# Kernel tuning notes

Hardware: AMD Instinct MI355X
Metric: run time of the kernel (lower is better)

The kernel has to match this reference:

```python
import jax, jax.numpy as jnp
import numpy as np

B, T, I, H, O = 4096, 256, 16, 32, 1


def setup_inputs() -> dict:
    key = jax.random.key(0)
    ks = jax.random.split(key, 8)
    s_ih = 1.0 / np.sqrt(H)
    x = jax.random.normal(ks[0], (B, T, I), dtype=jnp.float32)
    # PyTorch nn.LSTM params: gate order [i, f, g, o], uniform(-1/sqrt(H), 1/sqrt(H))
    W_ih = jax.random.uniform(ks[1], (4 * H, I), minval=-s_ih, maxval=s_ih, dtype=jnp.float32)
    W_hh = jax.random.uniform(ks[2], (4 * H, H), minval=-s_ih, maxval=s_ih, dtype=jnp.float32)
    b_ih = jax.random.uniform(ks[3], (4 * H,), minval=-s_ih, maxval=s_ih, dtype=jnp.float32)
    b_hh = jax.random.uniform(ks[4], (4 * H,), minval=-s_ih, maxval=s_ih, dtype=jnp.float32)
    W_fc = jax.random.uniform(ks[5], (O, H), minval=-s_ih, maxval=s_ih, dtype=jnp.float32)
    b_fc = jax.random.uniform(ks[6], (O,), minval=-s_ih, maxval=s_ih, dtype=jnp.float32)
    return {"x": x, "W_ih": W_ih, "W_hh": W_hh, "b_ih": b_ih, "b_hh": b_hh,
            "W_fc": W_fc, "b_fc": b_fc}


def _lstm_last_hidden(x, W_ih, W_hh, b_ih, b_hh):
    # Precompute input contributions for all timesteps: [T, B, 4H]
    xg = (jnp.einsum('bti,gi->btg', x, W_ih) + b_ih + b_hh).transpose(1, 0, 2)
    h0 = jnp.zeros((x.shape[0], W_hh.shape[1]), dtype=x.dtype)
    c0 = jnp.zeros_like(h0)

    def step(carry, xg_t):
        h, c = carry
        gates = xg_t + h @ W_hh.T  # [B, 4H]
        i, f, g, o = jnp.split(gates, 4, axis=-1)
        i = jax.nn.sigmoid(i)
        f = jax.nn.sigmoid(f)
        g = jnp.tanh(g)
        o = jax.nn.sigmoid(o)
        c = f * c + i * g
        h = o * jnp.tanh(c)
        return (h, c), None

    (h_last, _), _ = jax.lax.scan(step, (h0, c0), xg)
    return h_last


def reference(x, W_ih, W_hh, b_ih, b_hh, W_fc, b_fc):
    h_last = _lstm_last_hidden(x, W_ih, W_hh, b_ih, b_hh)
    # Dropout is identity in eval mode
    return h_last @ W_fc.T + b_fc  # [B, O]
```

## Files before the change

### kernel.cpp

```cpp
#include <hip/hip_runtime.h>

#define B_ 4096
#define T_ 256
#define I_ 16
#define H_ 32

typedef _Float16 f16x4 __attribute__((ext_vector_type(4)));
typedef _Float16 f16x8 __attribute__((ext_vector_type(8)));
typedef float    f32x4 __attribute__((ext_vector_type(4)));

#define MSIG  (-1.442695041f)
#define MTANH (-2.885390082f)

__global__ __launch_bounds__(128, 1)
void lstm_mfma2(const float* __restrict__ x,
                const float* __restrict__ Wih,
                const float* __restrict__ Whh,
                const float* __restrict__ bih,
                const float* __restrict__ bhh,
                const float* __restrict__ Wfc,
                const float* __restrict__ bfc,
                float* __restrict__ out)
{
    __shared__ __align__(16) _Float16 hbuf[2][16][40];

    const int tid  = threadIdx.x;
    const int wave = tid >> 6;
    const int l    = tid & 63;
    const int lr   = l & 15;
    const int lg   = l >> 4;
    const int b0   = blockIdx.x * 16;

    f16x8 whhA[4];
    f16x8 wihA[4];
    float mb[4][4];
#pragma unroll
    for (int q = 0; q < 4; ++q) {
        const int rowA = q * 32 + wave * 16 + lr;
        const float* ph = Whh + rowA * H_ + lg * 8;
#pragma unroll
        for (int k = 0; k < 8; ++k) whhA[q][k] = (_Float16)ph[k];
        const float* pi = Wih + rowA * I_ + (lg & 1) * 8;
#pragma unroll
        for (int k = 0; k < 8; ++k)
            wihA[q][k] = (lg < 2) ? (_Float16)pi[k] : (_Float16)0.0f;
        const float m = (q == 2) ? MTANH : MSIG;
#pragma unroll
        for (int r = 0; r < 4; ++r) {
            const int rowC = q * 32 + wave * 16 + lg * 4 + r;
            mb[q][r] = m * (bih[rowC] + bhh[rowC]);
        }
    }

    for (int i = tid; i < 2 * 16 * 40; i += 128)
        ((_Float16*)hbuf)[i] = (_Float16)0.0f;
    __syncthreads();

    float c0 = 0.f, c1 = 0.f, c2 = 0.f, c3 = 0.f;

    const float* xbase = x + (size_t)(b0 + lr) * (T_ * I_) + (lg & 1) * 8;
    f16x8 xf[8];
#pragma unroll
    for (int k = 0; k < 8; ++k) {
        const float4 u0 = *reinterpret_cast<const float4*>(xbase + k * I_);
        const float4 u1 = *reinterpret_cast<const float4*>(xbase + k * I_ + 4);
        f16x8 w;
        w[0] = (_Float16)u0.x; w[1] = (_Float16)u0.y;
        w[2] = (_Float16)u0.z; w[3] = (_Float16)u0.w;
        w[4] = (_Float16)u1.x; w[5] = (_Float16)u1.y;
        w[6] = (_Float16)u1.z; w[7] = (_Float16)u1.w;
        xf[k] = w;
    }

    const f32x4 zf = {0.f, 0.f, 0.f, 0.f};

    for (int tb = 0; tb < 32; ++tb) {
#pragma unroll
        for (int tt = 0; tt < 8; ++tt) {
            const f16x8 xB = xf[tt];
            if (tb < 31) {
                const float* nx = xbase + ((tb + 1) * 8 + tt) * I_;
                const float4 u0 = *reinterpret_cast<const float4*>(nx);
                const float4 u1 = *reinterpret_cast<const float4*>(nx + 4);
                f16x8 w;
                w[0] = (_Float16)u0.x; w[1] = (_Float16)u0.y;
                w[2] = (_Float16)u0.z; w[3] = (_Float16)u0.w;
                w[4] = (_Float16)u1.x; w[5] = (_Float16)u1.y;
                w[6] = (_Float16)u1.z; w[7] = (_Float16)u1.w;
                xf[tt] = w;
            }

            const f16x8 hB = *reinterpret_cast<const f16x8*>(&hbuf[tt & 1][lr][lg * 8]);

            f32x4 a0 = __builtin_amdgcn_mfma_f32_16x16x32_f16(wihA[0], xB, zf, 0, 0, 0);
            f32x4 a1 = __builtin_amdgcn_mfma_f32_16x16x32_f16(wihA[1], xB, zf, 0, 0, 0);
            f32x4 a2 = __builtin_amdgcn_mfma_f32_16x16x32_f16(wihA[2], xB, zf, 0, 0, 0);
            f32x4 a3 = __builtin_amdgcn_mfma_f32_16x16x32_f16(wihA[3], xB, zf, 0, 0, 0);
            a0 = __builtin_amdgcn_mfma_f32_16x16x32_f16(whhA[0], hB, a0, 0, 0, 0);
            a1 = __builtin_amdgcn_mfma_f32_16x16x32_f16(whhA[1], hB, a1, 0, 0, 0);
            a2 = __builtin_amdgcn_mfma_f32_16x16x32_f16(whhA[2], hB, a2, 0, 0, 0);
            a3 = __builtin_amdgcn_mfma_f32_16x16x32_f16(whhA[3], hB, a3, 0, 0, 0);

            float si[4], sf[4], tg[4], so[4];
#pragma unroll
            for (int r = 0; r < 4; ++r) {
                si[r] = __builtin_amdgcn_rcpf(1.0f + __builtin_amdgcn_exp2f(__fmaf_rn(MSIG,  a0[r], mb[0][r])));
                sf[r] = __builtin_amdgcn_rcpf(1.0f + __builtin_amdgcn_exp2f(__fmaf_rn(MSIG,  a1[r], mb[1][r])));
                tg[r] = __fmaf_rn(2.0f, __builtin_amdgcn_rcpf(1.0f + __builtin_amdgcn_exp2f(__fmaf_rn(MTANH, a2[r], mb[2][r]))), -1.0f);
                so[r] = __builtin_amdgcn_rcpf(1.0f + __builtin_amdgcn_exp2f(__fmaf_rn(MSIG,  a3[r], mb[3][r])));
            }

            c0 = __fmaf_rn(sf[0], c0, si[0] * tg[0]);
            c1 = __fmaf_rn(sf[1], c1, si[1] * tg[1]);
            c2 = __fmaf_rn(sf[2], c2, si[2] * tg[2]);
            c3 = __fmaf_rn(sf[3], c3, si[3] * tg[3]);
            const float t0 = __fmaf_rn(2.0f, __builtin_amdgcn_rcpf(1.0f + __builtin_amdgcn_exp2f(MTANH * c0)), -1.0f);
            const float t1 = __fmaf_rn(2.0f, __builtin_amdgcn_rcpf(1.0f + __builtin_amdgcn_exp2f(MTANH * c1)), -1.0f);
            const float t2 = __fmaf_rn(2.0f, __builtin_amdgcn_rcpf(1.0f + __builtin_amdgcn_exp2f(MTANH * c2)), -1.0f);
            const float t3 = __fmaf_rn(2.0f, __builtin_amdgcn_rcpf(1.0f + __builtin_amdgcn_exp2f(MTANH * c3)), -1.0f);
            const float h0 = so[0] * t0, h1 = so[1] * t1, h2 = so[2] * t2, h3 = so[3] * t3;

            f16x4 hv;
            hv[0] = (_Float16)h0; hv[1] = (_Float16)h1;
            hv[2] = (_Float16)h2; hv[3] = (_Float16)h3;
            *reinterpret_cast<f16x4*>(&hbuf[(tt + 1) & 1][lr][wave * 16 + lg * 4]) = hv;

            __syncthreads();
        }
    }

    if (tid < 64) {
        const f16x8 hL = *reinterpret_cast<const f16x8*>(&hbuf[0][lr][lg * 8]);
        const float* pw = Wfc + lg * 8;
        float p = 0.f;
#pragma unroll
        for (int k = 0; k < 8; ++k) p += (float)hL[k] * pw[k];
        p += __shfl_xor(p, 16, 64);
        p += __shfl_xor(p, 32, 64);
        if (lg == 0) out[b0 + lr] = p + bfc[0];
    }
}

extern "C" void kernel_launch(void* const* d_in, const int* in_sizes, int n_in,
                              void* d_out, int out_size, void* d_ws, size_t ws_size,
                              hipStream_t stream) {
    const float* x   = (const float*)d_in[0];
    const float* Wih = (const float*)d_in[1];
    const float* Whh = (const float*)d_in[2];
    const float* bih = (const float*)d_in[3];
    const float* bhh = (const float*)d_in[4];
    const float* Wfc = (const float*)d_in[5];
    const float* bfc = (const float*)d_in[6];
    float* out = (float*)d_out;

    dim3 grid(B_ / 16);
    dim3 block(128);
    hipLaunchKernelGGL(lstm_mfma2, grid, block, 0, stream,
                       x, Wih, Whh, bih, bhh, Wfc, bfc, out);
}
```

Before: 265.5 us.

## Run each LSTM batch tile in one wave, keeping hidden state in registers

Each block now has a single wave that computes all 128 gate rows for 16 batch elements. The gate rows are permuted so that the MFMA output layout matches the B-operand layout of the next step's h. This removes the shared-memory hidden buffer and the per-timestep __syncthreads. The bias is also folded into the MFMA accumulator initialisation. In exchange each wave issues twice the MFMAs and activation math per step, and the block count per CU halves in thread terms, which could lengthen the serial per-step critical path.

```diff
diff --git a/kernel.cpp b/kernel.cpp
--- a/kernel.cpp
+++ b/kernel.cpp
@@ -5,74 +5,85 @@
 #define I_ 16
 #define H_ 32
 
-typedef _Float16 f16x4 __attribute__((ext_vector_type(4)));
 typedef _Float16 f16x8 __attribute__((ext_vector_type(8)));
 typedef float    f32x4 __attribute__((ext_vector_type(4)));
 
 #define MSIG  (-1.442695041f)
 #define MTANH (-2.885390082f)
 
-__global__ __launch_bounds__(128, 1)
-void lstm_mfma2(const float* __restrict__ x,
-                const float* __restrict__ Wih,
-                const float* __restrict__ Whh,
-                const float* __restrict__ bih,
-                const float* __restrict__ bhh,
-                const float* __restrict__ Wfc,
-                const float* __restrict__ bfc,
-                float* __restrict__ out)
+__device__ __forceinline__ float sigm_(float a) {
+    return __builtin_amdgcn_rcpf(1.0f + __builtin_amdgcn_exp2f(MSIG * a));
+}
+__device__ __forceinline__ float tanh_(float a) {
+    return __fmaf_rn(2.0f, __builtin_amdgcn_rcpf(1.0f + __builtin_amdgcn_exp2f(MTANH * a)), -1.0f);
+}
+
+__global__ __launch_bounds__(64, 1)
+void lstm_wave(const float* __restrict__ x,
+               const float* __restrict__ Wih,
+               const float* __restrict__ Whh,
+               const float* __restrict__ bih,
+               const float* __restrict__ bhh,
+               const float* __restrict__ Wfc,
+               const float* __restrict__ bfc,
+               float* __restrict__ out)
 {
-    __shared__ __align__(16) _Float16 hbuf[2][16][40];
+    const int l  = threadIdx.x & 63;
+    const int lr = l & 15;
+    const int lg = l >> 4;
+    const int b0 = blockIdx.x * 16;
 
-    const int tid  = threadIdx.x;
-    const int wave = tid >> 6;
-    const int l    = tid & 63;
-    const int lr   = l & 15;
-    const int lg   = l >> 4;
-    const int b0   = blockIdx.x * 16;
-
-    f16x8 whhA[4];
-    f16x8 wihA[4];
-    float mb[4][4];
+    f16x8 whhA[4][2];
+    f16x8 wihA[4][2];
+    f32x4 biasC[4][2];
+    const int jA0 = ((lr >> 2) * 8) + (lr & 3);
 #pragma unroll
     for (int q = 0; q < 4; ++q) {
-        const int rowA = q * 32 + wave * 16 + lr;
-        const float* ph = Whh + rowA * H_ + lg * 8;
 #pragma unroll
-        for (int k = 0; k < 8; ++k) whhA[q][k] = (_Float16)ph[k];
-        const float* pi = Wih + rowA * I_ + (lg & 1) * 8;
+        for (int p = 0; p < 2; ++p) {
+            const int row = q * 32 + jA0 + p * 4;
+            const float* ph = Whh + row * H_ + lg * 8;
+            f16x8 w;
 #pragma unroll
-        for (int k = 0; k < 8; ++k)
-            wihA[q][k] = (lg < 2) ? (_Float16)pi[k] : (_Float16)0.0f;
-        const float m = (q == 2) ? MTANH : MSIG;
+            for (int k = 0; k < 8; ++k) w[k] = (_Float16)ph[k];
+            whhA[q][p] = w;
+            const float* pi = Wih + row * I_ + (lg & 1) * 8;
+            f16x8 wi;
 #pragma unroll
-        for (int r = 0; r < 4; ++r) {
-            const int rowC = q * 32 + wave * 16 + lg * 4 + r;
-            mb[q][r] = m * (bih[rowC] + bhh[rowC]);
+            for (int k = 0; k < 8; ++k)
+                wi[k] = (lg < 2) ? (_Float16)pi[k] : (_Float16)0.0f;
+            wihA[q][p] = wi;
+            f32x4 bc;
+#pragma unroll
+            for (int r = 0; r < 4; ++r) {
+                const int jC = lg * 8 + p * 4 + r;
+                bc[r] = bih[q * 32 + jC] + bhh[q * 32 + jC];
+            }
+            biasC[q][p] = bc;
         }
     }
-
-    for (int i = tid; i < 2 * 16 * 40; i += 128)
-        ((_Float16*)hbuf)[i] = (_Float16)0.0f;
-    __syncthreads();
-
-    float c0 = 0.f, c1 = 0.f, c2 = 0.f, c3 = 0.f;
 
     const float* xbase = x + (size_t)(b0 + lr) * (T_ * I_) + (lg & 1) * 8;
     f16x8 xf[8];
 #pragma unroll
-    for (int k = 0; k < 8; ++k) {
-        const float4 u0 = *reinterpret_cast<const float4*>(xbase + k * I_);
-        const float4 u1 = *reinterpret_cast<const float4*>(xbase + k * I_ + 4);
+    for (int t = 0; t < 8; ++t) {
+        const float4 u0 = *reinterpret_cast<const float4*>(xbase + t * I_);
+        const float4 u1 = *reinterpret_cast<const float4*>(xbase + t * I_ + 4);
         f16x8 w;
         w[0] = (_Float16)u0.x; w[1] = (_Float16)u0.y;
         w[2] = (_Float16)u0.z; w[3] = (_Float16)u0.w;
         w[4] = (_Float16)u1.x; w[5] = (_Float16)u1.y;
         w[6] = (_Float16)u1.z; w[7] = (_Float16)u1.w;
-        xf[k] = w;
+        xf[t] = w;
     }
 
-    const f32x4 zf = {0.f, 0.f, 0.f, 0.f};
+    f16x8 hB;
+#pragma unroll
+    for (int k = 0; k < 8; ++k) hB[k] = (_Float16)0.0f;
+    f32x4 cc0 = {0.f, 0.f, 0.f, 0.f};
+    f32x4 cc1 = {0.f, 0.f, 0.f, 0.f};
+    f32x4 hE = {0.f, 0.f, 0.f, 0.f};
+    f32x4 hO = {0.f, 0.f, 0.f, 0.f};
 
     for (int tb = 0; tb < 32; ++tb) {
 #pragma unroll
@@ -90,55 +101,52 @@
                 xf[tt] = w;
             }
 
-            const f16x8 hB = *reinterpret_cast<const f16x8*>(&hbuf[tt & 1][lr][lg * 8]);
+            f32x4 aQ[4][2];
+#pragma unroll
+            for (int q = 0; q < 4; ++q)
+#pragma unroll
+                for (int p = 0; p < 2; ++p)
+                    aQ[q][p] = __builtin_amdgcn_mfma_f32_16x16x32_f16(wihA[q][p], xB, biasC[q][p], 0, 0, 0);
+#pragma unroll
+            for (int q = 0; q < 4; ++q)
+#pragma unroll
+                for (int p = 0; p < 2; ++p)
+                    aQ[q][p] = __builtin_amdgcn_mfma_f32_16x16x32_f16(whhA[q][p], hB, aQ[q][p], 0, 0, 0);
 
-            f32x4 a0 = __builtin_amdgcn_mfma_f32_16x16x32_f16(wihA[0], xB, zf, 0, 0, 0);
-            f32x4 a1 = __builtin_amdgcn_mfma_f32_16x16x32_f16(wihA[1], xB, zf, 0, 0, 0);
-            f32x4 a2 = __builtin_amdgcn_mfma_f32_16x16x32_f16(wihA[2], xB, zf, 0, 0, 0);
-            f32x4 a3 = __builtin_amdgcn_mfma_f32_16x16x32_f16(wihA[3], xB, zf, 0, 0, 0);
-            a0 = __builtin_amdgcn_mfma_f32_16x16x32_f16(whhA[0], hB, a0, 0, 0, 0);
-            a1 = __builtin_amdgcn_mfma_f32_16x16x32_f16(whhA[1], hB, a1, 0, 0, 0);
-            a2 = __builtin_amdgcn_mfma_f32_16x16x32_f16(whhA[2], hB, a2, 0, 0, 0);
-            a3 = __builtin_amdgcn_mfma_f32_16x16x32_f16(whhA[3], hB, a3, 0, 0, 0);
-
-            float si[4], sf[4], tg[4], so[4];
 #pragma unroll
             for (int r = 0; r < 4; ++r) {
-                si[r] = __builtin_amdgcn_rcpf(1.0f + __builtin_amdgcn_exp2f(__fmaf_rn(MSIG,  a0[r], mb[0][r])));
-                sf[r] = __builtin_amdgcn_rcpf(1.0f + __builtin_amdgcn_exp2f(__fmaf_rn(MSIG,  a1[r], mb[1][r])));
-                tg[r] = __fmaf_rn(2.0f, __builtin_amdgcn_rcpf(1.0f + __builtin_amdgcn_exp2f(__fmaf_rn(MTANH, a2[r], mb[2][r]))), -1.0f);
-                so[r] = __builtin_amdgcn_rcpf(1.0f + __builtin_amdgcn_exp2f(__fmaf_rn(MSIG,  a3[r], mb[3][r])));
+                const float i0 = sigm_(aQ[0][0][r]);
+                const float f0 = sigm_(aQ[1][0][r]);
+                const float g0 = tanh_(aQ[2][0][r]);
+                const float o0 = sigm_(aQ[3][0][r]);
+                cc0[r] = __fmaf_rn(f0, cc0[r], i0 * g0);
+                hE[r]  = o0 * tanh_(cc0[r]);
+                const float i1 = sigm_(aQ[0][1][r]);
+                const float f1 = sigm_(aQ[1][1][r]);
+                const float g1 = tanh_(aQ[2][1][r]);
+                const float o1 = sigm_(aQ[3][1][r]);
+                cc1[r] = __fmaf_rn(f1, cc1[r], i1 * g1);
+                hO[r]  = o1 * tanh_(cc1[r]);
             }
 
-            c0 = __fmaf_rn(sf[0], c0, si[0] * tg[0]);
-            c1 = __fmaf_rn(sf[1], c1, si[1] * tg[1]);
-            c2 = __fmaf_rn(sf[2], c2, si[2] * tg[2]);
-            c3 = __fmaf_rn(sf[3], c3, si[3] * tg[3]);
-            const float t0 = __fmaf_rn(2.0f, __builtin_amdgcn_rcpf(1.0f + __builtin_amdgcn_exp2f(MTANH * c0)), -1.0f);
-            const float t1 = __fmaf_rn(2.0f, __builtin_amdgcn_rcpf(1.0f + __builtin_amdgcn_exp2f(MTANH * c1)), -1.0f);
-            const float t2 = __fmaf_rn(2.0f, __builtin_amdgcn_rcpf(1.0f + __builtin_amdgcn_exp2f(MTANH * c2)), -1.0f);
-            const float t3 = __fmaf_rn(2.0f, __builtin_amdgcn_rcpf(1.0f + __builtin_amdgcn_exp2f(MTANH * c3)), -1.0f);
-            const float h0 = so[0] * t0, h1 = so[1] * t1, h2 = so[2] * t2, h3 = so[3] * t3;
-
-            f16x4 hv;
-            hv[0] = (_Float16)h0; hv[1] = (_Float16)h1;
-            hv[2] = (_Float16)h2; hv[3] = (_Float16)h3;
-            *reinterpret_cast<f16x4*>(&hbuf[(tt + 1) & 1][lr][wave * 16 + lg * 4]) = hv;
-
-            __syncthreads();
+            f16x8 nh;
+#pragma unroll
+            for (int r = 0; r < 4; ++r) {
+                nh[r]     = (_Float16)hE[r];
+                nh[4 + r] = (_Float16)hO[r];
+            }
+            hB = nh;
         }
     }
 
-    if (tid < 64) {
-        const f16x8 hL = *reinterpret_cast<const f16x8*>(&hbuf[0][lr][lg * 8]);
-        const float* pw = Wfc + lg * 8;
-        float p = 0.f;
+    const float* pw = Wfc + lg * 8;
+    float pacc = 0.f;
 #pragma unroll
-        for (int k = 0; k < 8; ++k) p += (float)hL[k] * pw[k];
-        p += __shfl_xor(p, 16, 64);
-        p += __shfl_xor(p, 32, 64);
-        if (lg == 0) out[b0 + lr] = p + bfc[0];
-    }
+    for (int r = 0; r < 4; ++r)
+        pacc += hE[r] * pw[r] + hO[r] * pw[4 + r];
+    pacc += __shfl_xor(pacc, 16, 64);
+    pacc += __shfl_xor(pacc, 32, 64);
+    if (lg == 0) out[b0 + lr] = pacc + bfc[0];
 }
 
 extern "C" void kernel_launch(void* const* d_in, const int* in_sizes, int n_in,
@@ -154,7 +162,7 @@
     float* out = (float*)d_out;
 
     dim3 grid(B_ / 16);
-    dim3 block(128);
-    hipLaunchKernelGGL(lstm_mfma2, grid, block, 0, stream,
+    dim3 block(64);
+    hipLaunchKernelGGL(lstm_wave, grid, block, 0, stream,
                        x, Wih, Whh, bih, bhh, Wfc, bfc, out);
 }
```

Result: slower. 320.4 us (+20.7%).
